# Kernel tuning notes

Measured on AMD Instinct MI355X. Metric: run time of the kernel, lower is better.

Reference implementation:

```python
import jax, jax.numpy as jnp
import numpy as np

N_NODES = 100000
N_EDGES = 1600000
N_FEAT = 128
N_HIDDEN = 128
N_CLASS = 64


def setup_inputs() -> dict:
    key = jax.random.key(0)
    ks = jax.random.split(key, 8)
    s = 0.05  # small init scale
    return {
        "x": jax.random.normal(ks[0], (N_NODES, N_FEAT), dtype=jnp.float32),
        "W_l1": jax.random.normal(ks[1], (N_FEAT, N_HIDDEN), dtype=jnp.float32) * s,
        "b_l1": jnp.zeros((N_HIDDEN,), dtype=jnp.float32),
        "W_r1": jax.random.normal(ks[2], (N_FEAT, N_HIDDEN), dtype=jnp.float32) * s,
        "W_l2": jax.random.normal(ks[3], (N_HIDDEN, N_CLASS), dtype=jnp.float32) * s,
        "b_l2": jnp.zeros((N_CLASS,), dtype=jnp.float32),
        "W_r2": jax.random.normal(ks[4], (N_HIDDEN, N_CLASS), dtype=jnp.float32) * s,
        "edge_index": jax.random.randint(ks[5], (2, N_EDGES), 0, N_NODES, dtype=jnp.int64)
        if jax.config.jax_enable_x64 else jax.random.randint(ks[5], (2, N_EDGES), 0, N_NODES, dtype=jnp.int32),
    }


def _sage_conv(h, Wl, bl, Wr, src, dst, n_nodes):
    # PyG SAGEConv, aggr='mean': out = lin_l(mean_j x_j) + lin_r(x_i)
    msg = h[src]                                                 # [E, d] gather
    sums = jax.ops.segment_sum(msg, dst, num_segments=n_nodes)  # [N, d] scatter-add
    cnt = jax.ops.segment_sum(jnp.ones((src.shape[0],), h.dtype), dst,
                              num_segments=n_nodes)             # in-degree
    agg = sums / jnp.maximum(cnt, 1.0)[:, None]                 # mean (0 for isolated)
    return agg @ Wl + bl + h @ Wr


def reference(x, W_l1, b_l1, W_r1, W_l2, b_l2, W_r2, edge_index):
    src, dst = edge_index[0], edge_index[1]
    n = x.shape[0]
    # layer 0: conv -> relu (dropout inactive in eval)
    h = jax.nn.relu(_sage_conv(x, W_l1, b_l1, W_r1, src, dst, n))
    # layer 1 (last, no output_layer): conv only
    return _sage_conv(h, W_l2, b_l2, W_r2, src, dst, n)
```

## Files before the change

### kernel.cpp

```cpp
#include <hip/hip_runtime.h>
#include <cstddef>
#include <cstdint>


#define NC 391
#define CSH 8
#define CNODES 256
#define CCAP 4480
#define NT1 16
#define NT2 8

typedef __attribute__((ext_vector_type(4))) float f32x4;
typedef __attribute__((ext_vector_type(2))) float f32x2;
typedef __attribute__((ext_vector_type(8))) short bf16x8;

static __device__ __forceinline__ unsigned short f2bf(float f) {
    unsigned u = __float_as_uint(f);
    u += 0x7fffu + ((u >> 16) & 1u);
    return (unsigned short)(u >> 16);
}
static __device__ __forceinline__ float bflo(unsigned u) { return __uint_as_float(u << 16); }
static __device__ __forceinline__ float bfhi(unsigned u) { return __uint_as_float(u & 0xffff0000u); }

static __device__ __forceinline__ unsigned pk4fp8(float a, float b, float c, float d) {
    int v = 0;
    v = __builtin_amdgcn_cvt_pk_fp8_f32(a, b, v, false);
    v = __builtin_amdgcn_cvt_pk_fp8_f32(c, d, v, true);
    return (unsigned)v;
}

__global__ __launch_bounds__(256) void k_prep(
    const float* __restrict__ Wl1, const float* __restrict__ Wr1,
    const float* __restrict__ Wl2, const float* __restrict__ Wr2,
    unsigned short* __restrict__ B1, unsigned short* __restrict__ B2,
    int* __restrict__ ccnt) {
    int gid = blockIdx.x * 256 + threadIdx.x;
    if (gid >= 6144) {
        int i = gid - 6144;
        if (i < NC) ccnt[i] = 0;
        return;
    }
    const float* W;
    int col, kb, c;
    unsigned short* dst;
    int stride;
    if (gid < 4096) {
        int ks = gid >> 10, rem = gid & 1023, ct = rem >> 6, l = rem & 63;
        col = ct * 16 + (l & 15);
        kb = ks * 32 + ((l >> 4) << 3);
        W = col < 128 ? Wl1 : Wr1;
        c = col < 128 ? col : col - 128;
        stride = 128;
        dst = B1 + (size_t)gid * 8;
    } else {
        int g2 = gid - 4096;
        int ks = g2 >> 9, rem = g2 & 511, ct = rem >> 6, l = rem & 63;
        col = ct * 16 + (l & 15);
        kb = ks * 32 + ((l >> 4) << 3);
        W = col < 64 ? Wl2 : Wr2;
        c = col < 64 ? col : col - 64;
        stride = 64;
        dst = B2 + (size_t)g2 * 8;
    }
    unsigned v[4];
#pragma unroll
    for (int p = 0; p < 4; p++) {
        unsigned lo = f2bf(W[(size_t)(kb + 2 * p) * stride + c]);
        unsigned hi = f2bf(W[(size_t)(kb + 2 * p + 1) * stride + c]);
        v[p] = lo | (hi << 16);
    }
    *(uint4*)dst = *(uint4*)v;
}

__global__ __launch_bounds__(256) void k_phase1(
    const int* __restrict__ ei, int E,
    const float* __restrict__ x, const unsigned short* __restrict__ B1,
    int* __restrict__ ccnt, unsigned* __restrict__ bktc,
    unsigned char* __restrict__ xl8, unsigned short* __restrict__ xr,
    int M, int G_G, int G_B) {
    __shared__ unsigned short Bs[8192];
    __shared__ int cnt[NC], sbase[NC];
    int role = blockIdx.x & 1, idx = blockIdx.x >> 1;
    int tid = threadIdx.x;
    if (role == 1) {
        if (idx >= G_B) return;
        for (int i = tid; i < NC; i += 256) cnt[i] = 0;
        __syncthreads();
        unsigned pk[16];
        int cc[16], rr[16];
        int base_e = idx * 4096;
#pragma unroll
        for (int g = 0; g < 4; g++) {
            int e = base_e + (g * 256 + tid) * 4;
            if (e + 4 <= E) {
                int4 s4 = *(const int4*)(ei + e);
                int4 d4 = *(const int4*)(ei + (size_t)E + e);
                const int* sp = (const int*)&s4;
                const int* dp = (const int*)&d4;
#pragma unroll
                for (int j = 0; j < 4; j++) {
                    int k = g * 4 + j;
                    int dd = dp[j];
                    cc[k] = dd >> CSH;
                    pk[k] = (unsigned)sp[j] | (((unsigned)dd & 255u) << 17);
                    rr[k] = atomicAdd(&cnt[cc[k]], 1);
                }
            } else {
#pragma unroll
                for (int j = 0; j < 4; j++) {
                    int k = g * 4 + j;
                    int ee = e + j;
                    if (ee < E) {
                        int ss = ei[ee], dd = ei[(size_t)E + ee];
                        cc[k] = dd >> CSH;
                        pk[k] = (unsigned)ss | (((unsigned)dd & 255u) << 17);
                        rr[k] = atomicAdd(&cnt[cc[k]], 1);
                    } else cc[k] = -1;
                }
            }
        }
        __syncthreads();
        for (int i = tid; i < NC; i += 256)
            sbase[i] = atomicAdd(&ccnt[i], cnt[i]);
        __syncthreads();
#pragma unroll
        for (int k = 0; k < 16; k++) {
            if (cc[k] >= 0) {
                int pos = sbase[cc[k]] + rr[k];
                if (pos < CCAP) bktc[(size_t)cc[k] * CCAP + pos] = pk[k];
            }
        }
    } else {
        if (idx >= G_G) return;
        int wave = tid >> 6, lane = tid & 63;
        int row0 = idx * 64;
        int xrow = row0 + wave * 16 + (lane & 15);
        int xrc = xrow < M ? xrow : M - 1;
        const float* xp = x + (size_t)xrc * 128 + ((lane >> 4) << 3);
        f32x4 acc[NT1] = {};
        for (int ks = 0; ks < 4; ks++) {
            __syncthreads();
            {
                const uint4* src = (const uint4*)(B1 + (size_t)ks * 8192);
                uint4* dst = (uint4*)Bs;
#pragma unroll
                for (int it = 0; it < 4; it++)
                    dst[it * 256 + tid] = src[it * 256 + tid];
            }
            __syncthreads();
            float4 a0 = *(const float4*)(xp + ks * 32);
            float4 a1 = *(const float4*)(xp + ks * 32 + 4);
            bf16x8 xb;
            xb[0] = (short)f2bf(a0.x); xb[1] = (short)f2bf(a0.y);
            xb[2] = (short)f2bf(a0.z); xb[3] = (short)f2bf(a0.w);
            xb[4] = (short)f2bf(a1.x); xb[5] = (short)f2bf(a1.y);
            xb[6] = (short)f2bf(a1.z); xb[7] = (short)f2bf(a1.w);
#pragma unroll
            for (int ct = 0; ct < NT1; ct++) {
                bf16x8 wf = *(const bf16x8*)&Bs[((ct << 6) + lane) << 3];
                acc[ct] = __builtin_amdgcn_mfma_f32_16x16x32_bf16(
                    wf, xb, acc[ct], 0, 0, 0);
            }
        }
        if (xrow < M) {
#pragma unroll
            for (int ct = 0; ct < NT1; ct++) {
                int colb = (ct & 7) * 16 + ((lane >> 4) << 2);
                if (ct < 8) {
                    unsigned pv = pk4fp8(acc[ct][0], acc[ct][1],
                                         acc[ct][2], acc[ct][3]);
                    *(unsigned*)(xl8 + (size_t)xrow * 128 + colb) = pv;
                } else {
                    ushort4 o;
                    o.x = f2bf(acc[ct][0]); o.y = f2bf(acc[ct][1]);
                    o.z = f2bf(acc[ct][2]); o.w = f2bf(acc[ct][3]);
                    *(ushort4*)(xr + (size_t)xrow * 128 + colb) = o;
                }
            }
        }
    }
}

__global__ __launch_bounds__(256) void k_sort(
    const int* __restrict__ ccnt, unsigned* __restrict__ bktc,
    int* __restrict__ deg, int* __restrict__ rowb, int n) {
    __shared__ unsigned buf[CCAP];
    __shared__ unsigned short rank[CCAP];
    __shared__ int cnt[CNODES];
    __shared__ int base[CNODES];
    __shared__ int wsum[4];
    int b = blockIdx.x, tid = threadIdx.x;
    cnt[tid] = 0;
    __syncthreads();
    int ne = min(ccnt[b], CCAP);
    unsigned* seg = bktc + (size_t)b * CCAP;
    for (int i = tid; i < ne; i += 256) {
        unsigned pk = seg[i];
        buf[i] = pk;
        rank[i] = (unsigned short)atomicAdd(&cnt[pk >> 17], 1);
    }
    __syncthreads();
    {
        int v = cnt[tid];
        int lane = tid & 63, wid = tid >> 6;
        int sv = v;
#pragma unroll
        for (int d = 1; d < 64; d <<= 1) {
            int t = __shfl_up(sv, d);
            if (lane >= d) sv += t;
        }
        if (lane == 63) wsum[wid] = sv;
        __syncthreads();
        int wb = 0;
#pragma unroll
        for (int w = 0; w < 4; w++) if (w < wid) wb += wsum[w];
        base[tid] = wb + sv - v;
    }
    __syncthreads();
    for (int i = tid; i < ne; i += 256) {
        unsigned pk = buf[i];
        int dl = (int)(pk >> 17);
        seg[base[dl] + rank[i]] = pk & 0x1ffffu;
    }
    {
        int node = (b << CSH) + tid;
        if (node < n) {
            deg[node] = cnt[tid];
            rowb[node] = b * CCAP + base[tid];
        }
    }
}

__global__ __launch_bounds__(256) void k_aggB(
    const unsigned char* __restrict__ xl8, const unsigned short* __restrict__ xr,
    const float* __restrict__ b1,
    const int* __restrict__ deg, const int* __restrict__ rowb,
    const unsigned* __restrict__ sorted,
    unsigned short* __restrict__ hb, int n) {
    int gw = (int)((blockIdx.x * 256u + threadIdx.x) >> 4);
    int l16 = threadIdx.x & 15;
    if (gw >= n) return;
    int c = deg[gw];
    const unsigned* seg = sorted + rowb[gw];
    const uint2* xlu = (const uint2*)xl8;
    float a0 = 0.f, a1 = 0.f, a2 = 0.f, a3 = 0.f;
    float a4 = 0.f, a5 = 0.f, a6 = 0.f, a7 = 0.f;
#define ACC8(u)                                                              \
    {                                                                        \
        f32x2 p0 = __builtin_amdgcn_cvt_pk_f32_fp8((int)(u).x, false);       \
        f32x2 p1 = __builtin_amdgcn_cvt_pk_f32_fp8((int)(u).x, true);        \
        f32x2 p2 = __builtin_amdgcn_cvt_pk_f32_fp8((int)(u).y, false);       \
        f32x2 p3 = __builtin_amdgcn_cvt_pk_f32_fp8((int)(u).y, true);        \
        a0 += p0[0]; a1 += p0[1]; a2 += p1[0]; a3 += p1[1];                  \
        a4 += p2[0]; a5 += p2[1]; a6 += p3[0]; a7 += p3[1];                  \
    }
    int e = 0;
    for (; e + 8 <= c; e += 8) {
        unsigned s0 = seg[e + 0], s1 = seg[e + 1], s2 = seg[e + 2], s3 = seg[e + 3];
        unsigned s4 = seg[e + 4], s5 = seg[e + 5], s6 = seg[e + 6], s7 = seg[e + 7];
        uint2 u0 = xlu[(size_t)s0 * 16 + l16], u1 = xlu[(size_t)s1 * 16 + l16];
        uint2 u2 = xlu[(size_t)s2 * 16 + l16], u3 = xlu[(size_t)s3 * 16 + l16];
        uint2 u4 = xlu[(size_t)s4 * 16 + l16], u5 = xlu[(size_t)s5 * 16 + l16];
        uint2 u6 = xlu[(size_t)s6 * 16 + l16], u7 = xlu[(size_t)s7 * 16 + l16];
        ACC8(u0) ACC8(u1) ACC8(u2) ACC8(u3)
        ACC8(u4) ACC8(u5) ACC8(u6) ACC8(u7)
    }
    for (; e + 4 <= c; e += 4) {
        unsigned s0 = seg[e + 0], s1 = seg[e + 1], s2 = seg[e + 2], s3 = seg[e + 3];
        uint2 u0 = xlu[(size_t)s0 * 16 + l16], u1 = xlu[(size_t)s1 * 16 + l16];
        uint2 u2 = xlu[(size_t)s2 * 16 + l16], u3 = xlu[(size_t)s3 * 16 + l16];
        ACC8(u0) ACC8(u1) ACC8(u2) ACC8(u3)
    }
    for (; e < c; e++) {
        uint2 u = xlu[(size_t)seg[e] * 16 + l16];
        ACC8(u)
    }
#undef ACC8
    float inv = (c > 0) ? 1.0f / (float)c : 0.f;
    float4 bbA = *(const float4*)(b1 + l16 * 8);
    float4 bbB = *(const float4*)(b1 + l16 * 8 + 4);
    uint4 xu = ((const uint4*)xr)[(size_t)gw * 16 + l16];
    float v0 = fmaxf(fmaf(a0, inv, bflo(xu.x) + bbA.x), 0.f);
    float v1 = fmaxf(fmaf(a1, inv, bfhi(xu.x) + bbA.y), 0.f);
    float v2 = fmaxf(fmaf(a2, inv, bflo(xu.y) + bbA.z), 0.f);
    float v3 = fmaxf(fmaf(a3, inv, bfhi(xu.y) + bbA.w), 0.f);
    float v4 = fmaxf(fmaf(a4, inv, bflo(xu.z) + bbB.x), 0.f);
    float v5 = fmaxf(fmaf(a5, inv, bfhi(xu.z) + bbB.y), 0.f);
    float v6 = fmaxf(fmaf(a6, inv, bflo(xu.w) + bbB.z), 0.f);
    float v7 = fmaxf(fmaf(a7, inv, bfhi(xu.w) + bbB.w), 0.f);
    uint4 o;
    o.x = (unsigned)f2bf(v0) | ((unsigned)f2bf(v1) << 16);
    o.y = (unsigned)f2bf(v2) | ((unsigned)f2bf(v3) << 16);
    o.z = (unsigned)f2bf(v4) | ((unsigned)f2bf(v5) << 16);
    o.w = (unsigned)f2bf(v6) | ((unsigned)f2bf(v7) << 16);
    ((uint4*)hb)[(size_t)gw * 16 + l16] = o;
}

__global__ __launch_bounds__(256) void k_gemm2(
    const unsigned short* __restrict__ hb, const unsigned short* __restrict__ B2,
    unsigned char* __restrict__ hl28, unsigned short* __restrict__ hr2, int M) {
    __shared__ unsigned short Bs[4096];
    int tid = threadIdx.x, wave = tid >> 6, lane = tid & 63;
    int row0 = blockIdx.x * 64;
    int xrow = row0 + wave * 16 + (lane & 15);
    int xrc = xrow < M ? xrow : M - 1;
    const unsigned short* hp = hb + (size_t)xrc * 128 + ((lane >> 4) << 3);
    f32x4 acc[NT2] = {};
    for (int ks = 0; ks < 4; ks++) {
        __syncthreads();
        {
            const uint4* src = (const uint4*)(B2 + (size_t)ks * 4096);
            uint4* dst = (uint4*)Bs;
#pragma unroll
            for (int it = 0; it < 2; it++)
                dst[it * 256 + tid] = src[it * 256 + tid];
        }
        __syncthreads();
        bf16x8 xb = *(const bf16x8*)(hp + ks * 32);
#pragma unroll
        for (int ct = 0; ct < NT2; ct++) {
            bf16x8 wf = *(const bf16x8*)&Bs[((ct << 6) + lane) << 3];
            acc[ct] = __builtin_amdgcn_mfma_f32_16x16x32_bf16(
                wf, xb, acc[ct], 0, 0, 0);
        }
    }
    if (xrow < M) {
#pragma unroll
        for (int ct = 0; ct < NT2; ct++) {
            int colb = (ct & 3) * 16 + ((lane >> 4) << 2);
            if (ct < 4) {
                unsigned pv = pk4fp8(acc[ct][0], acc[ct][1],
                                     acc[ct][2], acc[ct][3]);
                *(unsigned*)(hl28 + (size_t)xrow * 64 + colb) = pv;
            } else {
                ushort4 o;
                o.x = f2bf(acc[ct][0]); o.y = f2bf(acc[ct][1]);
                o.z = f2bf(acc[ct][2]); o.w = f2bf(acc[ct][3]);
                *(ushort4*)(hr2 + (size_t)xrow * 64 + colb) = o;
            }
        }
    }
}

__global__ __launch_bounds__(256) void k_aggD(
    const unsigned char* __restrict__ hl28, const unsigned short* __restrict__ hr2,
    const float* __restrict__ b2,
    const int* __restrict__ deg, const int* __restrict__ rowb,
    const unsigned* __restrict__ sorted,
    float* __restrict__ out, int n) {
    int hw = (int)((blockIdx.x * 256u + threadIdx.x) >> 3);
    int l8 = threadIdx.x & 7;
    if (hw >= n) return;
    int c = deg[hw];
    const unsigned* seg = sorted + rowb[hw];
    const uint2* hu = (const uint2*)hl28;
    float a0 = 0.f, a1 = 0.f, a2 = 0.f, a3 = 0.f;
    float a4 = 0.f, a5 = 0.f, a6 = 0.f, a7 = 0.f;
#define ACC8(u)                                                              \
    {                                                                        \
        f32x2 p0 = __builtin_amdgcn_cvt_pk_f32_fp8((int)(u).x, false);       \
        f32x2 p1 = __builtin_amdgcn_cvt_pk_f32_fp8((int)(u).x, true);        \
        f32x2 p2 = __builtin_amdgcn_cvt_pk_f32_fp8((int)(u).y, false);       \
        f32x2 p3 = __builtin_amdgcn_cvt_pk_f32_fp8((int)(u).y, true);        \
        a0 += p0[0]; a1 += p0[1]; a2 += p1[0]; a3 += p1[1];                  \
        a4 += p2[0]; a5 += p2[1]; a6 += p3[0]; a7 += p3[1];                  \
    }
    int e = 0;
    for (; e + 8 <= c; e += 8) {
        unsigned s0 = seg[e + 0], s1 = seg[e + 1], s2 = seg[e + 2], s3 = seg[e + 3];
        unsigned s4 = seg[e + 4], s5 = seg[e + 5], s6 = seg[e + 6], s7 = seg[e + 7];
        uint2 u0 = hu[(size_t)s0 * 8 + l8], u1 = hu[(size_t)s1 * 8 + l8];
        uint2 u2 = hu[(size_t)s2 * 8 + l8], u3 = hu[(size_t)s3 * 8 + l8];
        uint2 u4 = hu[(size_t)s4 * 8 + l8], u5 = hu[(size_t)s5 * 8 + l8];
        uint2 u6 = hu[(size_t)s6 * 8 + l8], u7 = hu[(size_t)s7 * 8 + l8];
        ACC8(u0) ACC8(u1) ACC8(u2) ACC8(u3)
        ACC8(u4) ACC8(u5) ACC8(u6) ACC8(u7)
    }
    for (; e + 4 <= c; e += 4) {
        unsigned s0 = seg[e + 0], s1 = seg[e + 1], s2 = seg[e + 2], s3 = seg[e + 3];
        uint2 u0 = hu[(size_t)s0 * 8 + l8], u1 = hu[(size_t)s1 * 8 + l8];
        uint2 u2 = hu[(size_t)s2 * 8 + l8], u3 = hu[(size_t)s3 * 8 + l8];
        ACC8(u0) ACC8(u1) ACC8(u2) ACC8(u3)
    }
    for (; e < c; e++) {
        uint2 u = hu[(size_t)seg[e] * 8 + l8];
        ACC8(u)
    }
#undef ACC8
    float inv = (c > 0) ? 1.0f / (float)c : 0.f;
    float4 bbA = *(const float4*)(b2 + l8 * 8);
    float4 bbB = *(const float4*)(b2 + l8 * 8 + 4);
    uint4 ru = ((const uint4*)hr2)[(size_t)hw * 8 + l8];
    float4 oA, oB;
    oA.x = fmaf(a0, inv, bflo(ru.x) + bbA.x);
    oA.y = fmaf(a1, inv, bfhi(ru.x) + bbA.y);
    oA.z = fmaf(a2, inv, bflo(ru.y) + bbA.z);
    oA.w = fmaf(a3, inv, bfhi(ru.y) + bbA.w);
    oB.x = fmaf(a4, inv, bflo(ru.z) + bbB.x);
    oB.y = fmaf(a5, inv, bfhi(ru.z) + bbB.y);
    oB.z = fmaf(a6, inv, bflo(ru.w) + bbB.z);
    oB.w = fmaf(a7, inv, bfhi(ru.w) + bbB.w);
    *(float4*)(out + (size_t)hw * 64 + l8 * 8) = oA;
    *(float4*)(out + (size_t)hw * 64 + l8 * 8 + 4) = oB;
}

extern "C" void kernel_launch(void* const* d_in, const int* in_sizes, int n_in,
                              void* d_out, int out_size, void* d_ws, size_t ws_size,
                              hipStream_t stream) {
    const float* x   = (const float*)d_in[0];
    const float* Wl1 = (const float*)d_in[1];
    const float* bl1 = (const float*)d_in[2];
    const float* Wr1 = (const float*)d_in[3];
    const float* Wl2 = (const float*)d_in[4];
    const float* bl2 = (const float*)d_in[5];
    const float* Wr2 = (const float*)d_in[6];
    const int*   ei  = (const int*)d_in[7];
    const int N = in_sizes[0] / 128;
    const int E = in_sizes[7] / 2;

    auto align = [](size_t v) { return (v + 255) & ~(size_t)255; };
    char* p = (char*)d_ws;
    int* ccnt           = (int*)p;            p += align((size_t)NC * 4);
    unsigned* bktc      = (unsigned*)p;       p += align((size_t)NC * CCAP * 4);
    int* deg            = (int*)p;            p += align((size_t)N * 4);
    int* rowb           = (int*)p;            p += align((size_t)N * 4);
    unsigned short* B1  = (unsigned short*)p; p += align((size_t)4096 * 8 * 2);
    unsigned short* B2  = (unsigned short*)p; p += align((size_t)2048 * 8 * 2);
    unsigned char* xl8  = (unsigned char*)p;  p += align((size_t)N * 128);
    unsigned short* xr  = (unsigned short*)p; p += align((size_t)N * 128 * 2);
    unsigned short* hb  = (unsigned short*)p; p += align((size_t)N * 128 * 2);
    unsigned char* hl28 = xl8;
    unsigned short* hr2 = xr;

    const int G_G = (N + 63) / 64;
    const int G_B = (E + 4095) / 4096;
    const int G_MAX = G_G > G_B ? G_G : G_B;

    k_prep<<<26, 256, 0, stream>>>(Wl1, Wr1, Wl2, Wr2, B1, B2, ccnt);
    k_phase1<<<2 * G_MAX, 256, 0, stream>>>(ei, E, x, B1, ccnt, bktc,
                                            xl8, xr, N, G_G, G_B);
    k_sort<<<NC, 256, 0, stream>>>(ccnt, bktc, deg, rowb, N);
    k_aggB<<<(N * 16 + 255) / 256, 256, 0, stream>>>(xl8, xr, bl1, deg, rowb,
                                                     bktc, hb, N);
    k_gemm2<<<G_G, 256, 0, stream>>>(hb, B2, hl28, hr2, N);
    k_aggD<<<(N * 8 + 255) / 256, 256, 0, stream>>>(hl28, hr2, bl2, deg, rowb,
                                                    bktc, (float*)d_out, N);
}
```

Measured before the change: 162.7 us.

## Fuse layer-1 aggregation with layer-2 GEMM through shared memory

Merges the first-layer mean aggregation kernel and the second-layer projection GEMM into one kernel. Each block aggregates 64 nodes into a shared-memory tile of bf16 hidden features, then runs MFMA against B2, which is read directly from global memory. This removes the global write and re-read of the hidden activations and one kernel launch. The cost is fewer, larger blocks with a serial 4-node loop per thread group, which lowers the number of gathers in flight, plus a barrier before the GEMM. Outputs now go to separate buffers because the inputs can no longer be overwritten in place.

New measurement: 183.5 us. +12.8%, slower.

```diff
diff --git a/kernel.cpp b/kernel.cpp
--- a/kernel.cpp
+++ b/kernel.cpp
@@ -231,20 +231,17 @@
     }
 }
 
-__global__ __launch_bounds__(256) void k_aggB(
+__global__ __launch_bounds__(256) void k_aggBC(
     const unsigned char* __restrict__ xl8, const unsigned short* __restrict__ xr,
-    const float* __restrict__ b1,
+    const float* __restrict__ b1, const unsigned short* __restrict__ B2,
     const int* __restrict__ deg, const int* __restrict__ rowb,
     const unsigned* __restrict__ sorted,
-    unsigned short* __restrict__ hb, int n) {
-    int gw = (int)((blockIdx.x * 256u + threadIdx.x) >> 4);
-    int l16 = threadIdx.x & 15;
-    if (gw >= n) return;
-    int c = deg[gw];
-    const unsigned* seg = sorted + rowb[gw];
+    unsigned char* __restrict__ hl28, unsigned short* __restrict__ hr2, int n) {
+    __shared__ unsigned short hs[64][136];
+    int tid = threadIdx.x;
+    int base = blockIdx.x * 64;
+    int l16 = tid & 15, grp = tid >> 4;
     const uint2* xlu = (const uint2*)xl8;
-    float a0 = 0.f, a1 = 0.f, a2 = 0.f, a3 = 0.f;
-    float a4 = 0.f, a5 = 0.f, a6 = 0.f, a7 = 0.f;
 #define ACC8(u)                                                              \
     {                                                                        \
         f32x2 p0 = __builtin_amdgcn_cvt_pk_f32_fp8((int)(u).x, false);       \
@@ -254,77 +251,76 @@
         a0 += p0[0]; a1 += p0[1]; a2 += p1[0]; a3 += p1[1];                  \
         a4 += p2[0]; a5 += p2[1]; a6 += p3[0]; a7 += p3[1];                  \
     }
-    int e = 0;
-    for (; e + 8 <= c; e += 8) {
-        unsigned s0 = seg[e + 0], s1 = seg[e + 1], s2 = seg[e + 2], s3 = seg[e + 3];
-        unsigned s4 = seg[e + 4], s5 = seg[e + 5], s6 = seg[e + 6], s7 = seg[e + 7];
-        uint2 u0 = xlu[(size_t)s0 * 16 + l16], u1 = xlu[(size_t)s1 * 16 + l16];
-        uint2 u2 = xlu[(size_t)s2 * 16 + l16], u3 = xlu[(size_t)s3 * 16 + l16];
-        uint2 u4 = xlu[(size_t)s4 * 16 + l16], u5 = xlu[(size_t)s5 * 16 + l16];
-        uint2 u6 = xlu[(size_t)s6 * 16 + l16], u7 = xlu[(size_t)s7 * 16 + l16];
-        ACC8(u0) ACC8(u1) ACC8(u2) ACC8(u3)
-        ACC8(u4) ACC8(u5) ACC8(u6) ACC8(u7)
-    }
-    for (; e + 4 <= c; e += 4) {
-        unsigned s0 = seg[e + 0], s1 = seg[e + 1], s2 = seg[e + 2], s3 = seg[e + 3];
-        uint2 u0 = xlu[(size_t)s0 * 16 + l16], u1 = xlu[(size_t)s1 * 16 + l16];
-        uint2 u2 = xlu[(size_t)s2 * 16 + l16], u3 = xlu[(size_t)s3 * 16 + l16];
-        ACC8(u0) ACC8(u1) ACC8(u2) ACC8(u3)
-    }
-    for (; e < c; e++) {
-        uint2 u = xlu[(size_t)seg[e] * 16 + l16];
-        ACC8(u)
-    }
-#undef ACC8
-    float inv = (c > 0) ? 1.0f / (float)c : 0.f;
     float4 bbA = *(const float4*)(b1 + l16 * 8);
     float4 bbB = *(const float4*)(b1 + l16 * 8 + 4);
-    uint4 xu = ((const uint4*)xr)[(size_t)gw * 16 + l16];
-    float v0 = fmaxf(fmaf(a0, inv, bflo(xu.x) + bbA.x), 0.f);
-    float v1 = fmaxf(fmaf(a1, inv, bfhi(xu.x) + bbA.y), 0.f);
-    float v2 = fmaxf(fmaf(a2, inv, bflo(xu.y) + bbA.z), 0.f);
-    float v3 = fmaxf(fmaf(a3, inv, bfhi(xu.y) + bbA.w), 0.f);
-    float v4 = fmaxf(fmaf(a4, inv, bflo(xu.z) + bbB.x), 0.f);
-    float v5 = fmaxf(fmaf(a5, inv, bfhi(xu.z) + bbB.y), 0.f);
-    float v6 = fmaxf(fmaf(a6, inv, bflo(xu.w) + bbB.z), 0.f);
-    float v7 = fmaxf(fmaf(a7, inv, bfhi(xu.w) + bbB.w), 0.f);
-    uint4 o;
-    o.x = (unsigned)f2bf(v0) | ((unsigned)f2bf(v1) << 16);
-    o.y = (unsigned)f2bf(v2) | ((unsigned)f2bf(v3) << 16);
-    o.z = (unsigned)f2bf(v4) | ((unsigned)f2bf(v5) << 16);
-    o.w = (unsigned)f2bf(v6) | ((unsigned)f2bf(v7) << 16);
-    ((uint4*)hb)[(size_t)gw * 16 + l16] = o;
-}
-
-__global__ __launch_bounds__(256) void k_gemm2(
-    const unsigned short* __restrict__ hb, const unsigned short* __restrict__ B2,
-    unsigned char* __restrict__ hl28, unsigned short* __restrict__ hr2, int M) {
-    __shared__ unsigned short Bs[4096];
-    int tid = threadIdx.x, wave = tid >> 6, lane = tid & 63;
-    int row0 = blockIdx.x * 64;
-    int xrow = row0 + wave * 16 + (lane & 15);
-    int xrc = xrow < M ? xrow : M - 1;
-    const unsigned short* hp = hb + (size_t)xrc * 128 + ((lane >> 4) << 3);
+#pragma unroll 1
+    for (int it = 0; it < 4; it++) {
+        int dl = grp + it * 16;
+        int node = base + dl;
+        uint4 o = {0u, 0u, 0u, 0u};
+        if (node < n) {
+            int c = deg[node];
+            const unsigned* seg = sorted + rowb[node];
+            float a0 = 0.f, a1 = 0.f, a2 = 0.f, a3 = 0.f;
+            float a4 = 0.f, a5 = 0.f, a6 = 0.f, a7 = 0.f;
+            int e = 0;
+            for (; e + 8 <= c; e += 8) {
+                unsigned s0 = seg[e + 0], s1 = seg[e + 1];
+                unsigned s2 = seg[e + 2], s3 = seg[e + 3];
+                unsigned s4 = seg[e + 4], s5 = seg[e + 5];
+                unsigned s6 = seg[e + 6], s7 = seg[e + 7];
+                uint2 u0 = xlu[(size_t)s0 * 16 + l16], u1 = xlu[(size_t)s1 * 16 + l16];
+                uint2 u2 = xlu[(size_t)s2 * 16 + l16], u3 = xlu[(size_t)s3 * 16 + l16];
+                uint2 u4 = xlu[(size_t)s4 * 16 + l16], u5 = xlu[(size_t)s5 * 16 + l16];
+                uint2 u6 = xlu[(size_t)s6 * 16 + l16], u7 = xlu[(size_t)s7 * 16 + l16];
+                ACC8(u0) ACC8(u1) ACC8(u2) ACC8(u3)
+                ACC8(u4) ACC8(u5) ACC8(u6) ACC8(u7)
+            }
+            for (; e + 4 <= c; e += 4) {
+                unsigned s0 = seg[e + 0], s1 = seg[e + 1];
+                unsigned s2 = seg[e + 2], s3 = seg[e + 3];
+                uint2 u0 = xlu[(size_t)s0 * 16 + l16], u1 = xlu[(size_t)s1 * 16 + l16];
+                uint2 u2 = xlu[(size_t)s2 * 16 + l16], u3 = xlu[(size_t)s3 * 16 + l16];
+                ACC8(u0) ACC8(u1) ACC8(u2) ACC8(u3)
+            }
+            for (; e < c; e++) {
+                uint2 u = xlu[(size_t)seg[e] * 16 + l16];
+                ACC8(u)
+            }
+            float inv = (c > 0) ? 1.0f / (float)c : 0.f;
+            uint4 xu = ((const uint4*)xr)[(size_t)node * 16 + l16];
+            float v0 = fmaxf(fmaf(a0, inv, bflo(xu.x) + bbA.x), 0.f);
+            float v1 = fmaxf(fmaf(a1, inv, bfhi(xu.x) + bbA.y), 0.f);
+            float v2 = fmaxf(fmaf(a2, inv, bflo(xu.y) + bbA.z), 0.f);
+            float v3 = fmaxf(fmaf(a3, inv, bfhi(xu.y) + bbA.w), 0.f);
+            float v4 = fmaxf(fmaf(a4, inv, bflo(xu.z) + bbB.x), 0.f);
+            float v5 = fmaxf(fmaf(a5, inv, bfhi(xu.z) + bbB.y), 0.f);
+            float v6 = fmaxf(fmaf(a6, inv, bflo(xu.w) + bbB.z), 0.f);
+            float v7 = fmaxf(fmaf(a7, inv, bfhi(xu.w) + bbB.w), 0.f);
+            o.x = (unsigned)f2bf(v0) | ((unsigned)f2bf(v1) << 16);
+            o.y = (unsigned)f2bf(v2) | ((unsigned)f2bf(v3) << 16);
+            o.z = (unsigned)f2bf(v4) | ((unsigned)f2bf(v5) << 16);
+            o.w = (unsigned)f2bf(v6) | ((unsigned)f2bf(v7) << 16);
+        }
+        *(uint4*)&hs[dl][l16 * 8] = o;
+    }
+#undef ACC8
+    __syncthreads();
+    int wave = tid >> 6, lane = tid & 63;
+    int lrow = wave * 16 + (lane & 15);
+    int xrow = base + lrow;
     f32x4 acc[NT2] = {};
+#pragma unroll
     for (int ks = 0; ks < 4; ks++) {
-        __syncthreads();
-        {
-            const uint4* src = (const uint4*)(B2 + (size_t)ks * 4096);
-            uint4* dst = (uint4*)Bs;
-#pragma unroll
-            for (int it = 0; it < 2; it++)
-                dst[it * 256 + tid] = src[it * 256 + tid];
-        }
-        __syncthreads();
-        bf16x8 xb = *(const bf16x8*)(hp + ks * 32);
+        bf16x8 xb = *(const bf16x8*)&hs[lrow][((lane >> 4) << 3) + ks * 32];
 #pragma unroll
         for (int ct = 0; ct < NT2; ct++) {
-            bf16x8 wf = *(const bf16x8*)&Bs[((ct << 6) + lane) << 3];
+            bf16x8 wf = *(const bf16x8*)&B2[((size_t)(ks * 8 + ct) * 64 + lane) * 8];
             acc[ct] = __builtin_amdgcn_mfma_f32_16x16x32_bf16(
                 wf, xb, acc[ct], 0, 0, 0);
         }
     }
-    if (xrow < M) {
+    if (xrow < n) {
 #pragma unroll
         for (int ct = 0; ct < NT2; ct++) {
             int colb = (ct & 3) * 16 + ((lane >> 4) << 2);
@@ -428,9 +424,8 @@
     unsigned short* B2  = (unsigned short*)p; p += align((size_t)2048 * 8 * 2);
     unsigned char* xl8  = (unsigned char*)p;  p += align((size_t)N * 128);
     unsigned short* xr  = (unsigned short*)p; p += align((size_t)N * 128 * 2);
-    unsigned short* hb  = (unsigned short*)p; p += align((size_t)N * 128 * 2);
-    unsigned char* hl28 = xl8;
-    unsigned short* hr2 = xr;
+    unsigned char* hl28 = (unsigned char*)p;  p += align((size_t)N * 64);
+    unsigned short* hr2 = (unsigned short*)p; p += align((size_t)N * 64 * 2);
 
     const int G_G = (N + 63) / 64;
     const int G_B = (E + 4095) / 4096;
@@ -440,9 +435,8 @@
     k_phase1<<<2 * G_MAX, 256, 0, stream>>>(ei, E, x, B1, ccnt, bktc,
                                             xl8, xr, N, G_G, G_B);
     k_sort<<<NC, 256, 0, stream>>>(ccnt, bktc, deg, rowb, N);
-    k_aggB<<<(N * 16 + 255) / 256, 256, 0, stream>>>(xl8, xr, bl1, deg, rowb,
-                                                     bktc, hb, N);
-    k_gemm2<<<G_G, 256, 0, stream>>>(hb, B2, hl28, hr2, N);
+    k_aggBC<<<G_G, 256, 0, stream>>>(xl8, xr, bl1, B2, deg, rowb, bktc,
+                                     hl28, hr2, N);
     k_aggD<<<(N * 8 + 255) / 256, 256, 0, stream>>>(hl28, hr2, bl2, deg, rowb,
                                                     bktc, (float*)d_out, N);
 }
```
